# Kernel optimization log

Hardware: AMD Instinct MI355X
Metric: run time of the kernel (lower is better)

## Reference

```python
import jax, jax.numpy as jnp
import numpy as np

V, C, T = 4096, 32, 512


def setup_inputs() -> dict:
    key = jax.random.key(0)
    ks = jax.random.split(key, 6)
    return {
        "x": jax.random.normal(ks[0], (V, C, T), dtype=jnp.float32),
        "U_1": jax.random.normal(ks[1], (V,), dtype=jnp.float32),
        "U_2": jax.random.normal(ks[2], (C, V), dtype=jnp.float32),
        "U_3": jax.random.normal(ks[3], (C,), dtype=jnp.float32),
        "b_e": jax.random.normal(ks[4], (C, T, T), dtype=jnp.float32),
        "V_e": jax.random.normal(ks[5], (T, T), dtype=jnp.float32),
    }


def reference(x, U_1, U_2, U_3, b_e, V_e):
    # x: (V, C, T)
    # lhs = (x.permute(2,1,0) @ U_1) @ U_2  -> (T, C) @ (C, V) = (T, V)
    tmp = jnp.einsum("vct,v->tc", x, U_1)          # (T, C)
    lhs = tmp @ U_2                                   # (T, V)
    # rhs = x.permute(2,0,1) @ U_3 -> (T, V)
    rhs = jnp.einsum("vct,c->tv", x, U_3)           # (T, V)
    product = rhs @ lhs.T                             # (T, T)
    # sigmoid(product + b_e) broadcasts to (C, T, T); V_e @ ... -> (C, T, T)
    E = jnp.einsum("ts,csr->ctr", V_e, jax.nn.sigmoid(product + b_e))
    # max-subtract / exp / sum over dim 1 == softmax over axis 1
    return jax.nn.softmax(E, axis=1)
```

## Files before the change

kernel.cpp:

```cpp
#include <hip/hip_runtime.h>

#define V_N 4096
#define C_N 32
#define T_N 512
#define VCH 256

typedef float f32x4 __attribute__((ext_vector_type(4)));
typedef __bf16 bf16x4 __attribute__((ext_vector_type(4)));
typedef __bf16 bf16x8 __attribute__((ext_vector_type(8)));

__device__ inline f32x4 fma4(f32x4 a, float b, f32x4 c) {
    f32x4 r;
    r.x = fmaf(a.x, b, c.x); r.y = fmaf(a.y, b, c.y);
    r.z = fmaf(a.z, b, c.z); r.w = fmaf(a.w, b, c.w);
    return r;
}

__global__ __launch_bounds__(256, 1) void k_rt(const float* __restrict__ x,
                                               const float* __restrict__ U1,
                                               const float* __restrict__ U2,
                                               const float* __restrict__ U3,
                                               float* __restrict__ partT,
                                               float* __restrict__ partG) {
    __shared__ float xbuf[2][32][256];
    __shared__ f32x4 lsum[2][4][64];
    __shared__ float u2s[32][16];
    __shared__ float u1s[16];
    __shared__ float u3s[32];

    const int vc = blockIdx.x >> 1;
    const int half = blockIdx.x & 1;
    const int tid = threadIdx.x;
    const int w = tid >> 6;
    const int l = tid & 63;
    const int v0 = vc * 16;

    if (tid < 16) u1s[tid] = U1[v0 + tid];
    if (tid < 32) u3s[tid] = U3[tid];
    {
        int c = tid >> 3, e = tid & 7;
        u2s[c][e] = U2[(size_t)c * V_N + v0 + e];
        u2s[c][e + 8] = U2[(size_t)c * V_N + v0 + e + 8];
    }
    __syncthreads();

    float u3loc[8];
#pragma unroll
    for (int i = 0; i < 8; ++i) u3loc[i] = u3s[w * 8 + i];

    f32x4 accT[8], gacc[8];
#pragma unroll
    for (int i = 0; i < 8; ++i) { accT[i] = (f32x4)0.f; gacc[i] = (f32x4)0.f; }

    const float* xbase = x + (size_t)v0 * (C_N * T_N) + half * 256 + l * 4;

#define STAGE(vi) {                                                          \
    const float* xp_ = xbase + (size_t)(vi) * (C_N * T_N);                   \
    _Pragma("unroll")                                                        \
    for (int i_ = 0; i_ < 8; ++i_) {                                         \
        __builtin_amdgcn_global_load_lds(                                    \
            (const __attribute__((address_space(1))) void*)                  \
                (xp_ + (size_t)(w * 8 + i_) * T_N),                          \
            (__attribute__((address_space(3))) void*)                        \
                &xbuf[(vi) & 1][w * 8 + i_][0],                              \
            16, 0, 0);                                                       \
    } }

    STAGE(0);
#pragma unroll 1
    for (int vi = 0; vi < 16; ++vi) {
        const int buf = vi & 1;
        if (vi + 1 < 16) {
            STAGE(vi + 1);
            asm volatile("s_waitcnt vmcnt(8)" ::: "memory");
        } else {
            asm volatile("s_waitcnt vmcnt(0)" ::: "memory");
        }
        __builtin_amdgcn_sched_barrier(0);
        float u1 = u1s[vi];
        f32x4 racc = (f32x4)0.f;
#pragma unroll
        for (int i = 0; i < 8; ++i) {
            f32x4 xv = *(const f32x4*)&xbuf[buf][w * 8 + i][l * 4];
            accT[i] = fma4(xv, u1, accT[i]);
            racc = fma4(xv, u3loc[i], racc);
        }
        lsum[buf][w][l] = racc;
        asm volatile("s_waitcnt lgkmcnt(0)" ::: "memory");
        __builtin_amdgcn_sched_barrier(0);
        __builtin_amdgcn_s_barrier();
        f32x4 rhs = (lsum[buf][0][l] + lsum[buf][1][l]) +
                    (lsum[buf][2][l] + lsum[buf][3][l]);
#pragma unroll
        for (int i = 0; i < 8; ++i)
            gacc[i] = fma4(rhs, u2s[w * 8 + i][vi], gacc[i]);
    }
#undef STAGE

#pragma unroll
    for (int i = 0; i < 8; ++i) {
        size_t off = ((size_t)(w * 8 + i) * VCH + vc) * T_N + half * 256 + l * 4;
        *(f32x4*)&partT[off] = accT[i];
        *(f32x4*)&partG[off] = gacc[i];
    }
}

__global__ __launch_bounds__(128) void k_redpre(const float* __restrict__ partT,
                                                const float* __restrict__ partG,
                                                float* __restrict__ tmpT,
                                                float* __restrict__ Gc,
                                                const float* __restrict__ Ve,
                                                __bf16* __restrict__ VeHi,
                                                __bf16* __restrict__ VeLo) {
    if (blockIdx.x >= 512) {
        int o = ((blockIdx.x - 512) * 128 + threadIdx.x) * 4;
        int e0 = o & 7, lp = (o >> 3) & 63, tile = o >> 9;
        int kk = tile & 15, tt = tile >> 4;
        int t = tt * 16 + (lp & 15);
        int k = kk * 32 + (lp >> 4) * 8 + e0;
        f32x4 v = *(const f32x4*)&Ve[(size_t)t * T_N + k];
        bf16x4 h, lo;
#pragma unroll
        for (int j = 0; j < 4; ++j) {
            h[j] = (__bf16)v[j];
            lo[j] = (__bf16)(v[j] - (float)h[j]);
        }
        *(bf16x4*)&VeHi[o] = h;
        *(bf16x4*)&VeLo[o] = lo;
        return;
    }
    __shared__ f32x4 red[16][8];
    int oid = threadIdx.x & 15;
    int seg = threadIdx.x >> 4;
    int o = blockIdx.x * 16 + oid;
    int isG = o >> 12;
    int oo = o & 4095;
    int c = oo >> 7;
    int tq = oo & 127;
    const float* src = isG ? partG : partT;
    size_t base = (size_t)c * VCH * T_N + tq * 4;
    f32x4 s = (f32x4)0.f;
#pragma unroll 4
    for (int vc = seg * 32; vc < seg * 32 + 32; ++vc)
        s += *(const f32x4*)&src[base + (size_t)vc * T_N];
    red[oid][seg] = s;
    __syncthreads();
    if (seg == 0) {
        f32x4 tot = red[oid][0];
#pragma unroll
        for (int k = 1; k < 8; ++k) tot += red[oid][k];
        float* dst = isG ? Gc : tmpT;
        *(f32x4*)&dst[c * T_N + tq * 4] = tot;
    }
}

__global__ __launch_bounds__(256) void k_P2(const float* __restrict__ Gc,
                                            const float* __restrict__ tmpT,
                                            float* __restrict__ P) {
    __shared__ float Gs[32][64];
    __shared__ float Ts[32][64];
    int rbase = blockIdx.x * 64, sbase = blockIdx.y * 64;
    int tid = threadIdx.x;
    int tx = tid & 15, ty = tid >> 4;
    for (int i = tid; i < 2048; i += 256) {
        int cc = i >> 6, j = i & 63;
        Gs[cc][j] = Gc[cc * T_N + sbase + j];
        Ts[cc][j] = tmpT[cc * T_N + rbase + j];
    }
    __syncthreads();
    float acc[4][4] = {};
#pragma unroll
    for (int cc = 0; cc < 32; ++cc) {
        float a[4], b[4];
#pragma unroll
        for (int i = 0; i < 4; ++i) a[i] = Gs[cc][ty * 4 + i];
#pragma unroll
        for (int j = 0; j < 4; ++j) b[j] = Ts[cc][tx * 4 + j];
#pragma unroll
        for (int i = 0; i < 4; ++i)
#pragma unroll
            for (int j = 0; j < 4; ++j) acc[i][j] = fmaf(a[i], b[j], acc[i][j]);
    }
#pragma unroll
    for (int i = 0; i < 4; ++i) {
        f32x4 vv = {acc[i][0], acc[i][1], acc[i][2], acc[i][3]};
        *(f32x4*)&P[(size_t)(sbase + ty * 4 + i) * T_N + rbase + tx * 4] = vv;
    }
}

__global__ __launch_bounds__(512, 4) void k_fused(const float* __restrict__ P,
                                                  const float* __restrict__ be,
                                                  const __bf16* __restrict__ VeHi,
                                                  const __bf16* __restrict__ VeLo,
                                                  float* __restrict__ out) {
    __shared__ __bf16 S[32][512];
    const int rbase = blockIdx.x * 32;
    const int c = blockIdx.y;
    const int tid = threadIdx.x;
    const size_t cTT = (size_t)c * T_N * T_N;

    {
        int r4 = (tid & 7) * 4;
        int s0 = tid >> 3;
        for (int i = 0; i < 8; ++i) {
            int s = i * 64 + s0;
            size_t off = (size_t)s * T_N + rbase + r4;
            f32x4 pv = *(const f32x4*)&P[off];
            f32x4 bv = *(const f32x4*)&be[cTT + off];
#pragma unroll
            for (int j = 0; j < 4; ++j) {
                float vv = pv[j] + bv[j];
                float sg = 1.0f / (1.0f + __expf(-vv));
                int rl = r4 + j;
                S[rl][s ^ ((rl & 7) << 3)] = (__bf16)sg;
            }
        }
    }
    __syncthreads();

    const int lane = tid & 63;
    const int w = tid >> 6;
    const int lhi = lane >> 4;
    const int llo = lane & 15;

    const bf16x8* fragHi = (const bf16x8*)VeHi;
    const bf16x8* fragLo = (const bf16x8*)VeLo;

    f32x4 acc[4][2];
#pragma unroll
    for (int mi = 0; mi < 4; ++mi)
#pragma unroll
        for (int ni = 0; ni < 2; ++ni) acc[mi][ni] = (f32x4)0.f;

    for (int k0 = 0; k0 < T_N; k0 += 32) {
        bf16x8 b[2];
        int g = (k0 >> 3) + lhi;
#pragma unroll
        for (int ni = 0; ni < 2; ++ni) {
            int rr = ni * 16 + llo;
            b[ni] = *(const bf16x8*)&S[rr][(g ^ (rr & 7)) << 3];
        }
#pragma unroll
        for (int mi = 0; mi < 4; ++mi) {
            int tile = (w * 4 + mi) * 16 + (k0 >> 5);
            bf16x8 ah = fragHi[tile * 64 + lane];
            bf16x8 al = fragLo[tile * 64 + lane];
#pragma unroll
            for (int ni = 0; ni < 2; ++ni) {
                acc[mi][ni] = __builtin_amdgcn_mfma_f32_16x16x32_bf16(ah, b[ni], acc[mi][ni], 0, 0, 0);
                acc[mi][ni] = __builtin_amdgcn_mfma_f32_16x16x32_bf16(al, b[ni], acc[mi][ni], 0, 0, 0);
            }
        }
    }
    __syncthreads();

    float* red = (float*)&S[0][0];
    float gmax[2], gsum[2];

#pragma unroll
    for (int ni = 0; ni < 2; ++ni) {
        float m = -3.4e38f;
#pragma unroll
        for (int mi = 0; mi < 4; ++mi)
#pragma unroll
            for (int q = 0; q < 4; ++q) m = fmaxf(m, acc[mi][ni][q]);
        m = fmaxf(m, __shfl_xor(m, 16));
        m = fmaxf(m, __shfl_xor(m, 32));
        if (lane < 16) red[w * 32 + ni * 16 + llo] = m;
    }
    __syncthreads();
#pragma unroll
    for (int ni = 0; ni < 2; ++ni) {
        int col = ni * 16 + llo;
        float m = red[col];
#pragma unroll
        for (int wv = 1; wv < 8; ++wv) m = fmaxf(m, red[wv * 32 + col]);
        gmax[ni] = m;
    }
#pragma unroll
    for (int ni = 0; ni < 2; ++ni) {
        float ssum = 0.f;
#pragma unroll
        for (int mi = 0; mi < 4; ++mi)
#pragma unroll
            for (int q = 0; q < 4; ++q) {
                float e = __expf(acc[mi][ni][q] - gmax[ni]);
                acc[mi][ni][q] = e;
                ssum += e;
            }
        ssum += __shfl_xor(ssum, 16);
        ssum += __shfl_xor(ssum, 32);
        if (lane < 16) red[256 + w * 32 + ni * 16 + llo] = ssum;
    }
    __syncthreads();
#pragma unroll
    for (int ni = 0; ni < 2; ++ni) {
        int col = ni * 16 + llo;
        float s = red[256 + col];
#pragma unroll
        for (int wv = 1; wv < 8; ++wv) s += red[256 + wv * 32 + col];
        gsum[ni] = 1.0f / s;
    }
#pragma unroll
    for (int mi = 0; mi < 4; ++mi)
#pragma unroll
        for (int ni = 0; ni < 2; ++ni) {
            int rg = rbase + ni * 16 + llo;
#pragma unroll
            for (int q = 0; q < 4; ++q) {
                int t = w * 64 + mi * 16 + lhi * 4 + q;
                out[cTT + (size_t)t * T_N + rg] = acc[mi][ni][q] * gsum[ni];
            }
        }
}

extern "C" void kernel_launch(void* const* d_in, const int* in_sizes, int n_in,
                              void* d_out, int out_size, void* d_ws, size_t ws_size,
                              hipStream_t stream) {
    const float* x  = (const float*)d_in[0];
    const float* U1 = (const float*)d_in[1];
    const float* U2 = (const float*)d_in[2];
    const float* U3 = (const float*)d_in[3];
    const float* be = (const float*)d_in[4];
    const float* Ve = (const float*)d_in[5];
    float* out = (float*)d_out;

    float* ws    = (float*)d_ws;
    float* partT = ws;
    float* partG = ws + 4194304;
    float* P     = ws + 8388608;
    __bf16* VeHi = (__bf16*)(ws + 8650752);
    __bf16* VeLo = (__bf16*)(ws + 8781824);
    float* tmpT  = ws + 8912896;
    float* Gc    = ws + 8929280;

    k_rt    <<<512, 256, 0, stream>>>(x, U1, U2, U3, partT, partG);
    k_redpre<<<512 + 512, 128, 0, stream>>>(partT, partG, tmpT, Gc, Ve, VeHi, VeLo);
    k_P2    <<<dim3(8, 8), 256, 0, stream>>>(Gc, tmpT, P);
    k_fused <<<dim3(16, C_N), 512, 0, stream>>>(P, be, VeHi, VeLo, out);
}
```

Measured before the change: 105.4 us.

## Split k_rt over T into quarters with direct global loads and higher occupancy

The first pass over x now runs as 1024 blocks, each covering a quarter of T, instead of 512 blocks covering a half. Each thread handles 4 channels instead of 8, so register use drops and launch bounds allow 4 blocks per CU. The LDS double-buffered async staging (global_load_lds plus manual waitcnt) is replaced by plain vectorized global loads, relying on occupancy to hide latency. The cost is explicit prefetch overlap, in exchange for more waves in flight, and the cross-wave reduction now sums 8 LDS slots per iteration.

```diff
diff --git a/kernel.cpp b/kernel.cpp
--- a/kernel.cpp
+++ b/kernel.cpp
@@ -16,24 +16,26 @@
     return r;
 }
 
-__global__ __launch_bounds__(256, 1) void k_rt(const float* __restrict__ x,
+__global__ __launch_bounds__(256, 4) void k_rt(const float* __restrict__ x,
                                                const float* __restrict__ U1,
                                                const float* __restrict__ U2,
                                                const float* __restrict__ U3,
                                                float* __restrict__ partT,
                                                float* __restrict__ partG) {
-    __shared__ float xbuf[2][32][256];
-    __shared__ f32x4 lsum[2][4][64];
+    __shared__ f32x4 lsum[2][8][32];
     __shared__ float u2s[32][16];
     __shared__ float u1s[16];
     __shared__ float u3s[32];
 
-    const int vc = blockIdx.x >> 1;
-    const int half = blockIdx.x & 1;
+    const int vc = blockIdx.x >> 2;
+    const int q  = blockIdx.x & 3;
     const int tid = threadIdx.x;
     const int w = tid >> 6;
     const int l = tid & 63;
+    const int cs = l >> 5;
+    const int t4 = l & 31;
     const int v0 = vc * 16;
+    const int cbase = w * 8 + cs;
 
     if (tid < 16) u1s[tid] = U1[v0 + tid];
     if (tid < 32) u3s[tid] = U3[tid];
@@ -44,64 +46,44 @@
     }
     __syncthreads();
 
-    float u3loc[8];
-#pragma unroll
-    for (int i = 0; i < 8; ++i) u3loc[i] = u3s[w * 8 + i];
-
-    f32x4 accT[8], gacc[8];
-#pragma unroll
-    for (int i = 0; i < 8; ++i) { accT[i] = (f32x4)0.f; gacc[i] = (f32x4)0.f; }
-
-    const float* xbase = x + (size_t)v0 * (C_N * T_N) + half * 256 + l * 4;
-
-#define STAGE(vi) {                                                          \
-    const float* xp_ = xbase + (size_t)(vi) * (C_N * T_N);                   \
-    _Pragma("unroll")                                                        \
-    for (int i_ = 0; i_ < 8; ++i_) {                                         \
-        __builtin_amdgcn_global_load_lds(                                    \
-            (const __attribute__((address_space(1))) void*)                  \
-                (xp_ + (size_t)(w * 8 + i_) * T_N),                          \
-            (__attribute__((address_space(3))) void*)                        \
-                &xbuf[(vi) & 1][w * 8 + i_][0],                              \
-            16, 0, 0);                                                       \
-    } }
-
-    STAGE(0);
+    float u3loc[4];
+#pragma unroll
+    for (int j = 0; j < 4; ++j) u3loc[j] = u3s[cbase + j * 2];
+
+    f32x4 accT[4], gacc[4];
+#pragma unroll
+    for (int j = 0; j < 4; ++j) { accT[j] = (f32x4)0.f; gacc[j] = (f32x4)0.f; }
+
+    const float* xbase = x + (size_t)v0 * (C_N * T_N) + q * 128 + t4 * 4;
+
 #pragma unroll 1
     for (int vi = 0; vi < 16; ++vi) {
+        const float* xp = xbase + (size_t)vi * (C_N * T_N);
         const int buf = vi & 1;
-        if (vi + 1 < 16) {
-            STAGE(vi + 1);
-            asm volatile("s_waitcnt vmcnt(8)" ::: "memory");
-        } else {
-            asm volatile("s_waitcnt vmcnt(0)" ::: "memory");
-        }
-        __builtin_amdgcn_sched_barrier(0);
         float u1 = u1s[vi];
         f32x4 racc = (f32x4)0.f;
 #pragma unroll
-        for (int i = 0; i < 8; ++i) {
-            f32x4 xv = *(const f32x4*)&xbuf[buf][w * 8 + i][l * 4];
-            accT[i] = fma4(xv, u1, accT[i]);
-            racc = fma4(xv, u3loc[i], racc);
-        }
-        lsum[buf][w][l] = racc;
-        asm volatile("s_waitcnt lgkmcnt(0)" ::: "memory");
-        __builtin_amdgcn_sched_barrier(0);
-        __builtin_amdgcn_s_barrier();
-        f32x4 rhs = (lsum[buf][0][l] + lsum[buf][1][l]) +
-                    (lsum[buf][2][l] + lsum[buf][3][l]);
-#pragma unroll
-        for (int i = 0; i < 8; ++i)
-            gacc[i] = fma4(rhs, u2s[w * 8 + i][vi], gacc[i]);
-    }
-#undef STAGE
-
-#pragma unroll
-    for (int i = 0; i < 8; ++i) {
-        size_t off = ((size_t)(w * 8 + i) * VCH + vc) * T_N + half * 256 + l * 4;
-        *(f32x4*)&partT[off] = accT[i];
-        *(f32x4*)&partG[off] = gacc[i];
+        for (int j = 0; j < 4; ++j) {
+            f32x4 xv = *(const f32x4*)(xp + (size_t)(cbase + j * 2) * T_N);
+            accT[j] = fma4(xv, u1, accT[j]);
+            racc = fma4(xv, u3loc[j], racc);
+        }
+        lsum[buf][w * 2 + cs][t4] = racc;
+        __syncthreads();
+        f32x4 rhs = ((lsum[buf][0][t4] + lsum[buf][1][t4]) +
+                     (lsum[buf][2][t4] + lsum[buf][3][t4])) +
+                    ((lsum[buf][4][t4] + lsum[buf][5][t4]) +
+                     (lsum[buf][6][t4] + lsum[buf][7][t4]));
+#pragma unroll
+        for (int j = 0; j < 4; ++j)
+            gacc[j] = fma4(rhs, u2s[cbase + j * 2][vi], gacc[j]);
+    }
+
+#pragma unroll
+    for (int j = 0; j < 4; ++j) {
+        size_t off = ((size_t)(cbase + j * 2) * VCH + vc) * T_N + q * 128 + t4 * 4;
+        *(f32x4*)&partT[off] = accT[j];
+        *(f32x4*)&partG[off] = gacc[j];
     }
 }
 
@@ -334,7 +316,7 @@
     float* tmpT  = ws + 8912896;
     float* Gc    = ws + 8929280;
 
-    k_rt    <<<512, 256, 0, stream>>>(x, U1, U2, U3, partT, partG);
+    k_rt    <<<1024, 256, 0, stream>>>(x, U1, U2, U3, partT, partG);
     k_redpre<<<512 + 512, 128, 0, stream>>>(partT, partG, tmpT, Gc, Ve, VeHi, VeLo);
     k_P2    <<<dim3(8, 8), 256, 0, stream>>>(Gc, tmpT, P);
     k_fused <<<dim3(16, C_N), 512, 0, stream>>>(P, be, VeHi, VeLo, out);
```

Result: no change. 106.0 us (+0.5%).
